# Kernel tuning notes

Hardware: AMD Instinct MI355X
Metric: run time of the kernel (lower is better)

The kernel has to match this reference:

```python
import jax, jax.numpy as jnp
import numpy as np
from jax import lax

EPS = 1e-7  # keras K.epsilon()
DN = ('NHWC', 'HWIO', 'NHWC')


def _box_avg(z, k):
    """Depthwise k x k box filter with SAME padding, scaled by 1/(k*k*C).
    Matches tf.nn.depthwise_conv2d with a ones/(k*k*C) kernel, implemented
    separably (two 1D convs) for efficiency."""
    C = z.shape[-1]
    scale = 1.0 / (k * k * C)  # note: keras code divides by full kernel size incl. C
    kh = jnp.ones((k, 1, 1, C), z.dtype)
    kw = jnp.ones((1, k, 1, C), z.dtype)
    z = lax.conv_general_dilated(z, kh, (1, 1), 'SAME',
                                 dimension_numbers=DN, feature_group_count=C)
    z = lax.conv_general_dilated(z, kw, (1, 1), 'SAME',
                                 dimension_numbers=DN, feature_group_count=C)
    return z * scale


def setup_inputs() -> dict:
    key = jax.random.key(0)
    x = jax.random.normal(key, (8, 1024, 1024, 2), dtype=jnp.float32)
    return {"x": x, "filter_size": 61}


def reference(x, filter_size):
    k = int(filter_size)
    # norm_method == 'std':
    out = x - _box_avg(x, k)                       # local mean-subtract
    c1 = _box_avg(out, k)
    c2 = _box_avg(out * out, k)
    std = jnp.sqrt(c2 - c1 * c1) + EPS             # local window std
    return out / std
```

## Files before the change

### kernel.cpp

```cpp
#include <hip/hip_runtime.h>
#include <math.h>

#define NB 8
#define HH 1024
#define WW 1024
#define RAD 30
#define KS 61
#define ROWSZ 2048
#define IMGSZ (HH * ROWSZ)
#define STR2 1024
#define NCOL2 (NB * STR2)
#define VSEGH 32
#define VNSEG (HH / VSEGH)
#define EPSV 1e-7f
#define SCALEV (1.0f / (float)(KS * KS * 2))
#define PDW (WW + WW / 8)
#define PD(i) ((i) + ((i) >> 3))

__device__ __forceinline__ unsigned bf16_rn(float f) {
    unsigned u = __float_as_uint(f);
    return (u + 0x7FFFu + ((u >> 16) & 1u)) >> 16;
}
__device__ __forceinline__ unsigned pk2(float a, float b) {
    return bf16_rn(a) | (bf16_rn(b) << 16);
}
__device__ __forceinline__ float2 up2(unsigned u) {
    return make_float2(__uint_as_float(u << 16),
                       __uint_as_float(u & 0xFFFF0000u));
}

__device__ __forceinline__ float2 f2add(float2 a, float2 b) {
    return make_float2(a.x + b.x, a.y + b.y);
}
__device__ __forceinline__ float2 f2sub(float2 a, float2 b) {
    return make_float2(a.x - b.x, a.y - b.y);
}

__global__ __launch_bounds__(256, 2) void vbox_kernel(const float* __restrict__ in,
                                                      unsigned* __restrict__ out) {
    int tid = blockIdx.x * 256 + threadIdx.x;
    int col = tid & (NCOL2 - 1);
    int seg = tid >> 13;
    int n = col >> 10;
    int w2 = col & (STR2 - 1);
    const float2* ip = (const float2*)(in + (size_t)n * IMGSZ) + w2;
    unsigned* op = out + (size_t)n * (IMGSZ / 2) + w2;
    int h0 = seg * VSEGH;
    float2 S = make_float2(0.f, 0.f);
    int lo = h0 - RAD; if (lo < 0) lo = 0;
    int h = lo;
    for (; h + 8 <= h0 + RAD; h += 8) {
        float2 W[8];
        #pragma unroll
        for (int i = 0; i < 8; ++i) W[i] = ip[(h + i) * STR2];
        __builtin_amdgcn_sched_barrier(0);
        #pragma unroll
        for (int i = 0; i < 8; ++i) S = f2add(S, W[i]);
    }
    for (; h < h0 + RAD; ++h) S = f2add(S, ip[h * STR2]);

    if (seg != 0 && seg != VNSEG - 1) {
        const float2* lp = ip + (h0 + RAD) * STR2;
        const float2* tp = ip + (h0 - RAD) * STR2;
        unsigned* opp = op + (size_t)h0 * STR2;
        for (int r = 0; r < VSEGH; r += 8) {
            float2 L[8], T[8];
            #pragma unroll
            for (int i = 0; i < 8; ++i) L[i] = lp[(r + i) * STR2];
            #pragma unroll
            for (int i = 0; i < 8; ++i) T[i] = tp[(r + i) * STR2];
            __builtin_amdgcn_sched_barrier(0);
            #pragma unroll
            for (int i = 0; i < 8; ++i) {
                S = f2add(S, L[i]);
                opp[(r + i) * STR2] = pk2(S.x, S.y);
                S = f2sub(S, T[i]);
            }
        }
    } else {
        const float2 Z = make_float2(0.f, 0.f);
        for (int ho = h0; ho < h0 + VSEGH; ho += 4) {
            float2 a[4], b[4];
            #pragma unroll
            for (int i = 0; i < 4; ++i) {
                int ha = ho + i + RAD;
                a[i] = (ha < HH) ? ip[ha * STR2] : Z;
            }
            #pragma unroll
            for (int i = 0; i < 4; ++i) {
                int hb = ho + i - RAD;
                b[i] = (hb >= 0) ? ip[hb * STR2] : Z;
            }
            #pragma unroll
            for (int i = 0; i < 4; ++i) {
                S = f2add(S, a[i]);
                op[(size_t)(ho + i) * STR2] = pk2(S.x, S.y);
                S = f2sub(S, b[i]);
            }
        }
    }
}

__device__ inline float wave_incl_scan(float v) {
    int lane = threadIdx.x & 63;
    #pragma unroll
    for (int d = 1; d < 64; d <<= 1) {
        float o = __shfl_up(v, d, 64);
        if (lane >= d) v += o;
    }
    return v;
}

__global__ __launch_bounds__(256) void hmid_kernel(const unsigned* __restrict__ vsum,
                                                   const float* __restrict__ x,
                                                   float* __restrict__ out,
                                                   uint2* __restrict__ hig) {
    __shared__ float ch[2][PDW];
    __shared__ float s4[4][PDW];
    __shared__ float wtot[4];
    int t = threadIdx.x;
    size_t g = (size_t)blockIdx.x * ROWSZ;
    const uint4* vrow = (const uint4*)(vsum + (size_t)blockIdx.x * STR2);
    uint4 u = vrow[t];
    {
        float2 p0 = up2(u.x), p1 = up2(u.y), p2 = up2(u.z), p3 = up2(u.w);
        int w = 4 * t;
        ch[0][PD(w + 0)] = p0.x; ch[1][PD(w + 0)] = p0.y;
        ch[0][PD(w + 1)] = p1.x; ch[1][PD(w + 1)] = p1.y;
        ch[0][PD(w + 2)] = p2.x; ch[1][PD(w + 2)] = p2.y;
        ch[0][PD(w + 3)] = p3.x; ch[1][PD(w + 3)] = p3.y;
    }
    __syncthreads();
    {
        int c = t >> 7, j = t & 127, base = j * 8;
        float v[8]; float run = 0.f;
        #pragma unroll
        for (int i = 0; i < 8; ++i) { run += ch[c][PD(base + i)]; v[i] = run; }
        float incl = wave_incl_scan(run);
        int wid = t >> 6;
        if ((t & 63) == 63) wtot[wid] = incl;
        __syncthreads();
        float off = incl - run;
        if (wid & 1) off += wtot[wid - 1];
        #pragma unroll
        for (int i = 0; i < 8; ++i) ch[c][PD(base + i)] = off + v[i];
    }
    __syncthreads();
    const float4* xrow = (const float4*)(x + g);
    float4* orow = (float4*)(out + g);
    #pragma unroll
    for (int i = 0; i < 2; ++i) {
        int jj = t + 256 * i;
        int w0 = 2 * jj, w1 = 2 * jj + 1;
        int hi0 = w0 + RAD; if (hi0 > WW - 1) hi0 = WW - 1;
        int hi1 = w1 + RAD; if (hi1 > WW - 1) hi1 = WW - 1;
        int lo0 = w0 - RAD - 1, lo1 = w1 - RAD - 1;
        float s00 = ch[0][PD(hi0)], s10 = ch[1][PD(hi0)];
        if (lo0 >= 0) { s00 -= ch[0][PD(lo0)]; s10 -= ch[1][PD(lo0)]; }
        float s01 = ch[0][PD(hi1)], s11 = ch[1][PD(hi1)];
        if (lo1 >= 0) { s01 -= ch[0][PD(lo1)]; s11 -= ch[1][PD(lo1)]; }
        float4 xv = xrow[jj];
        float4 o;
        o.x = xv.x - SCALEV * s00; o.y = xv.y - SCALEV * s10;
        o.z = xv.z - SCALEV * s01; o.w = xv.w - SCALEV * s11;
        orow[jj] = o;
        s4[0][PD(w0)] = o.x;       s4[1][PD(w0)] = o.y;
        s4[0][PD(w1)] = o.z;       s4[1][PD(w1)] = o.w;
        s4[2][PD(w0)] = o.x * o.x; s4[3][PD(w0)] = o.y * o.y;
        s4[2][PD(w1)] = o.z * o.z; s4[3][PD(w1)] = o.w * o.w;
    }
    __syncthreads();
    {
        int a = t >> 6, j = t & 63, base = j * 16;
        float v[16]; float run = 0.f;
        #pragma unroll
        for (int i = 0; i < 16; ++i) { run += s4[a][PD(base + i)]; v[i] = run; }
        float incl = wave_incl_scan(run);
        float off = incl - run;
        #pragma unroll
        for (int i = 0; i < 16; ++i) s4[a][PD(base + i)] = off + v[i];
    }
    __syncthreads();
    uint4* hirow = (uint4*)(hig + (size_t)blockIdx.x * STR2);
    #pragma unroll
    for (int i = 0; i < 2; ++i) {
        int jj = t + 256 * i;
        int w0 = 2 * jj, w1 = 2 * jj + 1;
        int hi0 = w0 + RAD; if (hi0 > WW - 1) hi0 = WW - 1;
        int hi1 = w1 + RAD; if (hi1 > WW - 1) hi1 = WW - 1;
        int lo0 = w0 - RAD - 1, lo1 = w1 - RAD - 1;
        float a00 = s4[0][PD(hi0)], a10 = s4[1][PD(hi0)];
        float q00 = s4[2][PD(hi0)], q10 = s4[3][PD(hi0)];
        if (lo0 >= 0) {
            a00 -= s4[0][PD(lo0)]; a10 -= s4[1][PD(lo0)];
            q00 -= s4[2][PD(lo0)]; q10 -= s4[3][PD(lo0)];
        }
        float a01 = s4[0][PD(hi1)], a11 = s4[1][PD(hi1)];
        float q01 = s4[2][PD(hi1)], q11 = s4[3][PD(hi1)];
        if (lo1 >= 0) {
            a01 -= s4[0][PD(lo1)]; a11 -= s4[1][PD(lo1)];
            q01 -= s4[2][PD(lo1)]; q11 -= s4[3][PD(lo1)];
        }
        hirow[jj] = make_uint4(pk2(a00, a10), pk2(q00, q10),
                               pk2(a01, a11), pk2(q01, q11));
    }
}

__global__ __launch_bounds__(256, 2) void vfinal_kernel(const uint2* __restrict__ hi,
                                                        float* __restrict__ io) {
    int tid = blockIdx.x * 256 + threadIdx.x;
    int col = tid & (NCOL2 - 1);
    int seg = tid >> 13;
    int n = col >> 10;
    int w2 = col & (STR2 - 1);
    const uint2* pp = hi + (size_t)n * ((size_t)HH * STR2) + w2;
    float2* op = (float2*)(io + (size_t)n * IMGSZ) + w2;
    int h0 = seg * VSEGH;
    float2 S1 = make_float2(0.f, 0.f);
    float2 S2 = make_float2(0.f, 0.f);
    int lo = h0 - RAD; if (lo < 0) lo = 0;
    int h = lo;
    for (; h + 8 <= h0 + RAD; h += 8) {
        uint2 A[8];
        #pragma unroll
        for (int i = 0; i < 8; ++i) A[i] = pp[(h + i) * STR2];
        __builtin_amdgcn_sched_barrier(0);
        #pragma unroll
        for (int i = 0; i < 8; ++i) {
            S1 = f2add(S1, up2(A[i].x));
            S2 = f2add(S2, up2(A[i].y));
        }
    }
    for (; h < h0 + RAD; ++h) {
        uint2 v = pp[h * STR2];
        S1 = f2add(S1, up2(v.x));
        S2 = f2add(S2, up2(v.y));
    }

    if (seg != 0 && seg != VNSEG - 1) {
        const uint2* lp = pp + (h0 + RAD) * STR2;
        const uint2* tp = pp + (h0 - RAD) * STR2;
        float2* q = op + (size_t)h0 * STR2;
        for (int r = 0; r < VSEGH; r += 8) {
            uint2 L[8], T[8];
            float2 O[8];
            #pragma unroll
            for (int i = 0; i < 8; ++i) L[i] = lp[(r + i) * STR2];
            #pragma unroll
            for (int i = 0; i < 8; ++i) T[i] = tp[(r + i) * STR2];
            #pragma unroll
            for (int i = 0; i < 8; ++i) O[i] = q[(r + i) * STR2];
            __builtin_amdgcn_sched_barrier(0);
            #pragma unroll
            for (int i = 0; i < 8; ++i) {
                S1 = f2add(S1, up2(L[i].x));
                S2 = f2add(S2, up2(L[i].y));
                float c1x = SCALEV * S1.x, c1y = SCALEV * S1.y;
                float vx = fmaxf(SCALEV * S2.x - c1x * c1x, 0.f);
                float vy = fmaxf(SCALEV * S2.y - c1y * c1y, 0.f);
                float2 yv;
                yv.x = O[i].x / (sqrtf(vx) + EPSV);
                yv.y = O[i].y / (sqrtf(vy) + EPSV);
                q[(r + i) * STR2] = yv;
                S1 = f2sub(S1, up2(T[i].x));
                S2 = f2sub(S2, up2(T[i].y));
            }
        }
    } else {
        const uint2 Z2u = make_uint2(0u, 0u);
        for (int ho = h0; ho < h0 + VSEGH; ho += 4) {
            uint2 a[4], b[4];
            float2 O[4];
            #pragma unroll
            for (int i = 0; i < 4; ++i) {
                int ha = ho + i + RAD;
                a[i] = (ha < HH) ? pp[ha * STR2] : Z2u;
            }
            #pragma unroll
            for (int i = 0; i < 4; ++i) {
                int hb = ho + i - RAD;
                b[i] = (hb >= 0) ? pp[hb * STR2] : Z2u;
            }
            #pragma unroll
            for (int i = 0; i < 4; ++i) O[i] = op[(size_t)(ho + i) * STR2];
            #pragma unroll
            for (int i = 0; i < 4; ++i) {
                S1 = f2add(S1, up2(a[i].x));
                S2 = f2add(S2, up2(a[i].y));
                float c1x = SCALEV * S1.x, c1y = SCALEV * S1.y;
                float vx = fmaxf(SCALEV * S2.x - c1x * c1x, 0.f);
                float vy = fmaxf(SCALEV * S2.y - c1y * c1y, 0.f);
                float2 yv;
                yv.x = O[i].x / (sqrtf(vx) + EPSV);
                yv.y = O[i].y / (sqrtf(vy) + EPSV);
                op[(size_t)(ho + i) * STR2] = yv;
                S1 = f2sub(S1, up2(b[i].x));
                S2 = f2sub(S2, up2(b[i].y));
            }
        }
    }
}

extern "C" void kernel_launch(void* const* d_in, const int* in_sizes, int n_in,
                              void* d_out, int out_size, void* d_ws, size_t ws_size,
                              hipStream_t stream) {
    const float* x = (const float*)d_in[0];
    float* out = (float*)d_out;
    unsigned* V1 = (unsigned*)d_ws;
    uint2* HI = (uint2*)(V1 + (size_t)NB * IMGSZ / 2);

    int vgrid = (NCOL2 * VNSEG) / 256;
    vbox_kernel<<<vgrid, 256, 0, stream>>>(x, V1);
    hmid_kernel<<<NB * HH, 256, 0, stream>>>(V1, x, out, HI);
    vfinal_kernel<<<vgrid, 256, 0, stream>>>(HI, out);
}
```

Measured before the change: 208.9 us.

## Widen vertical box kernels to 16-byte accesses with double-buffered row loads

Both vertical running-sum kernels now handle two pixels (four channels) per thread using float4/uint4 loads and stores instead of 8-byte accesses, which halves the thread count. The interior path double-buffers 8-row batches so the next batch's loads are in flight while the current one is consumed. The final kernel also swaps the divide and sqrtf for the hardware rcp/sqrt builtins. The cost is more registers (launch_bounds minimum occupancy hint dropped) and fewer waves in flight, plus slightly lower precision from the approximate rcp/sqrt.

```diff
diff --git a/kernel.cpp b/kernel.cpp
--- a/kernel.cpp
+++ b/kernel.cpp
@@ -9,7 +9,8 @@
 #define ROWSZ 2048
 #define IMGSZ (HH * ROWSZ)
 #define STR2 1024
-#define NCOL2 (NB * STR2)
+#define STR4 512
+#define NCOL4 (NB * STR4)
 #define VSEGH 32
 #define VNSEG (HH / VSEGH)
 #define EPSV 1e-7f
@@ -28,74 +29,86 @@
     return make_float2(__uint_as_float(u << 16),
                        __uint_as_float(u & 0xFFFF0000u));
 }
-
 __device__ __forceinline__ float2 f2add(float2 a, float2 b) {
     return make_float2(a.x + b.x, a.y + b.y);
 }
 __device__ __forceinline__ float2 f2sub(float2 a, float2 b) {
     return make_float2(a.x - b.x, a.y - b.y);
 }
-
-__global__ __launch_bounds__(256, 2) void vbox_kernel(const float* __restrict__ in,
-                                                      unsigned* __restrict__ out) {
+__device__ __forceinline__ float sqrt_f(float x) { return __builtin_amdgcn_sqrtf(x); }
+__device__ __forceinline__ float rcp_f(float x)  { return __builtin_amdgcn_rcpf(x); }
+
+__global__ __launch_bounds__(256) void vbox_kernel(const float* __restrict__ in,
+                                                   unsigned* __restrict__ out) {
     int tid = blockIdx.x * 256 + threadIdx.x;
-    int col = tid & (NCOL2 - 1);
-    int seg = tid >> 13;
-    int n = col >> 10;
-    int w2 = col & (STR2 - 1);
-    const float2* ip = (const float2*)(in + (size_t)n * IMGSZ) + w2;
-    unsigned* op = out + (size_t)n * (IMGSZ / 2) + w2;
+    int col = tid & (NCOL4 - 1);
+    int seg = tid >> 12;
+    int n = col >> 9;
+    int c = col & (STR4 - 1);
+    const float4* ip = (const float4*)(in + (size_t)n * IMGSZ) + c;
+    uint2* op = (uint2*)(out + (size_t)n * (IMGSZ / 2)) + c;
     int h0 = seg * VSEGH;
-    float2 S = make_float2(0.f, 0.f);
+    float4 S = make_float4(0.f, 0.f, 0.f, 0.f);
     int lo = h0 - RAD; if (lo < 0) lo = 0;
     int h = lo;
     for (; h + 8 <= h0 + RAD; h += 8) {
-        float2 W[8];
-        #pragma unroll
-        for (int i = 0; i < 8; ++i) W[i] = ip[(h + i) * STR2];
+        float4 W[8];
+        #pragma unroll
+        for (int i = 0; i < 8; ++i) W[i] = ip[(h + i) * STR4];
         __builtin_amdgcn_sched_barrier(0);
         #pragma unroll
-        for (int i = 0; i < 8; ++i) S = f2add(S, W[i]);
-    }
-    for (; h < h0 + RAD; ++h) S = f2add(S, ip[h * STR2]);
+        for (int i = 0; i < 8; ++i) {
+            S.x += W[i].x; S.y += W[i].y; S.z += W[i].z; S.w += W[i].w;
+        }
+    }
+    for (; h < h0 + RAD; ++h) {
+        float4 w = ip[h * STR4];
+        S.x += w.x; S.y += w.y; S.z += w.z; S.w += w.w;
+    }
 
     if (seg != 0 && seg != VNSEG - 1) {
-        const float2* lp = ip + (h0 + RAD) * STR2;
-        const float2* tp = ip + (h0 - RAD) * STR2;
-        unsigned* opp = op + (size_t)h0 * STR2;
-        for (int r = 0; r < VSEGH; r += 8) {
-            float2 L[8], T[8];
-            #pragma unroll
-            for (int i = 0; i < 8; ++i) L[i] = lp[(r + i) * STR2];
-            #pragma unroll
-            for (int i = 0; i < 8; ++i) T[i] = tp[(r + i) * STR2];
-            __builtin_amdgcn_sched_barrier(0);
-            #pragma unroll
-            for (int i = 0; i < 8; ++i) {
-                S = f2add(S, L[i]);
-                opp[(r + i) * STR2] = pk2(S.x, S.y);
-                S = f2sub(S, T[i]);
-            }
-        }
+        const float4* lp = ip + (h0 + RAD) * STR4;
+        const float4* tp = ip + (h0 - RAD) * STR4;
+        uint2* opp = op + (size_t)h0 * STR4;
+        float4 LA[8], TA[8], LB[8], TB[8];
+#define VB_LOAD(Lx, Tx, r) { \
+        _Pragma("unroll") for (int i = 0; i < 8; ++i) Lx[i] = lp[((r) + i) * STR4]; \
+        _Pragma("unroll") for (int i = 0; i < 8; ++i) Tx[i] = tp[((r) + i) * STR4]; \
+        __builtin_amdgcn_sched_barrier(0); }
+#define VB_CONS(Lx, Tx, r) { \
+        _Pragma("unroll") for (int i = 0; i < 8; ++i) { \
+            S.x += Lx[i].x; S.y += Lx[i].y; S.z += Lx[i].z; S.w += Lx[i].w; \
+            opp[((r) + i) * STR4] = make_uint2(pk2(S.x, S.y), pk2(S.z, S.w)); \
+            S.x -= Tx[i].x; S.y -= Tx[i].y; S.z -= Tx[i].z; S.w -= Tx[i].w; } }
+        VB_LOAD(LA, TA, 0)
+        VB_LOAD(LB, TB, 8)
+        VB_CONS(LA, TA, 0)
+        VB_LOAD(LA, TA, 16)
+        VB_CONS(LB, TB, 8)
+        VB_LOAD(LB, TB, 24)
+        VB_CONS(LA, TA, 16)
+        VB_CONS(LB, TB, 24)
+#undef VB_LOAD
+#undef VB_CONS
     } else {
-        const float2 Z = make_float2(0.f, 0.f);
+        const float4 Z = make_float4(0.f, 0.f, 0.f, 0.f);
         for (int ho = h0; ho < h0 + VSEGH; ho += 4) {
-            float2 a[4], b[4];
+            float4 a[4], b[4];
             #pragma unroll
             for (int i = 0; i < 4; ++i) {
                 int ha = ho + i + RAD;
-                a[i] = (ha < HH) ? ip[ha * STR2] : Z;
+                a[i] = (ha < HH) ? ip[ha * STR4] : Z;
             }
             #pragma unroll
             for (int i = 0; i < 4; ++i) {
                 int hb = ho + i - RAD;
-                b[i] = (hb >= 0) ? ip[hb * STR2] : Z;
-            }
-            #pragma unroll
-            for (int i = 0; i < 4; ++i) {
-                S = f2add(S, a[i]);
-                op[(size_t)(ho + i) * STR2] = pk2(S.x, S.y);
-                S = f2sub(S, b[i]);
+                b[i] = (hb >= 0) ? ip[hb * STR4] : Z;
+            }
+            #pragma unroll
+            for (int i = 0; i < 4; ++i) {
+                S.x += a[i].x; S.y += a[i].y; S.z += a[i].z; S.w += a[i].w;
+                op[(size_t)(ho + i) * STR4] = make_uint2(pk2(S.x, S.y), pk2(S.z, S.w));
+                S.x -= b[i].x; S.y -= b[i].y; S.z -= b[i].z; S.w -= b[i].w;
             }
         }
     }
@@ -206,99 +219,99 @@
     }
 }
 
-__global__ __launch_bounds__(256, 2) void vfinal_kernel(const uint2* __restrict__ hi,
-                                                        float* __restrict__ io) {
+__global__ __launch_bounds__(256) void vfinal_kernel(const uint2* __restrict__ hi,
+                                                     float* __restrict__ io) {
     int tid = blockIdx.x * 256 + threadIdx.x;
-    int col = tid & (NCOL2 - 1);
-    int seg = tid >> 13;
-    int n = col >> 10;
-    int w2 = col & (STR2 - 1);
-    const uint2* pp = hi + (size_t)n * ((size_t)HH * STR2) + w2;
-    float2* op = (float2*)(io + (size_t)n * IMGSZ) + w2;
+    int col = tid & (NCOL4 - 1);
+    int seg = tid >> 12;
+    int n = col >> 9;
+    int c = col & (STR4 - 1);
+    const uint4* pp = (const uint4*)(hi + (size_t)n * (size_t)HH * STR2) + c;
+    float4* op = (float4*)(io + (size_t)n * IMGSZ) + c;
     int h0 = seg * VSEGH;
-    float2 S1 = make_float2(0.f, 0.f);
-    float2 S2 = make_float2(0.f, 0.f);
+    float2 S1a = make_float2(0.f, 0.f), S2a = make_float2(0.f, 0.f);
+    float2 S1b = make_float2(0.f, 0.f), S2b = make_float2(0.f, 0.f);
     int lo = h0 - RAD; if (lo < 0) lo = 0;
     int h = lo;
     for (; h + 8 <= h0 + RAD; h += 8) {
-        uint2 A[8];
-        #pragma unroll
-        for (int i = 0; i < 8; ++i) A[i] = pp[(h + i) * STR2];
+        uint4 A[8];
+        #pragma unroll
+        for (int i = 0; i < 8; ++i) A[i] = pp[(h + i) * STR4];
         __builtin_amdgcn_sched_barrier(0);
         #pragma unroll
         for (int i = 0; i < 8; ++i) {
-            S1 = f2add(S1, up2(A[i].x));
-            S2 = f2add(S2, up2(A[i].y));
+            S1a = f2add(S1a, up2(A[i].x)); S2a = f2add(S2a, up2(A[i].y));
+            S1b = f2add(S1b, up2(A[i].z)); S2b = f2add(S2b, up2(A[i].w));
         }
     }
     for (; h < h0 + RAD; ++h) {
-        uint2 v = pp[h * STR2];
-        S1 = f2add(S1, up2(v.x));
-        S2 = f2add(S2, up2(v.y));
-    }
+        uint4 v = pp[h * STR4];
+        S1a = f2add(S1a, up2(v.x)); S2a = f2add(S2a, up2(v.y));
+        S1b = f2add(S1b, up2(v.z)); S2b = f2add(S2b, up2(v.w));
+    }
+
+#define VF_ROW(Ai, Oi, Ti, ro) { \
+    S1a = f2add(S1a, up2((Ai).x)); S2a = f2add(S2a, up2((Ai).y)); \
+    S1b = f2add(S1b, up2((Ai).z)); S2b = f2add(S2b, up2((Ai).w)); \
+    float4 yv; \
+    yv.x = (Oi).x * rcp_f(sqrt_f(fmaxf(SCALEV * S2a.x - (SCALEV * S1a.x) * (SCALEV * S1a.x), 0.f)) + EPSV); \
+    yv.y = (Oi).y * rcp_f(sqrt_f(fmaxf(SCALEV * S2a.y - (SCALEV * S1a.y) * (SCALEV * S1a.y), 0.f)) + EPSV); \
+    yv.z = (Oi).z * rcp_f(sqrt_f(fmaxf(SCALEV * S2b.x - (SCALEV * S1b.x) * (SCALEV * S1b.x), 0.f)) + EPSV); \
+    yv.w = (Oi).w * rcp_f(sqrt_f(fmaxf(SCALEV * S2b.y - (SCALEV * S1b.y) * (SCALEV * S1b.y), 0.f)) + EPSV); \
+    oq[(ro) * STR4] = yv; \
+    S1a = f2sub(S1a, up2((Ti).x)); S2a = f2sub(S2a, up2((Ti).y)); \
+    S1b = f2sub(S1b, up2((Ti).z)); S2b = f2sub(S2b, up2((Ti).w)); \
+}
 
     if (seg != 0 && seg != VNSEG - 1) {
-        const uint2* lp = pp + (h0 + RAD) * STR2;
-        const uint2* tp = pp + (h0 - RAD) * STR2;
-        float2* q = op + (size_t)h0 * STR2;
-        for (int r = 0; r < VSEGH; r += 8) {
-            uint2 L[8], T[8];
-            float2 O[8];
-            #pragma unroll
-            for (int i = 0; i < 8; ++i) L[i] = lp[(r + i) * STR2];
-            #pragma unroll
-            for (int i = 0; i < 8; ++i) T[i] = tp[(r + i) * STR2];
-            #pragma unroll
-            for (int i = 0; i < 8; ++i) O[i] = q[(r + i) * STR2];
-            __builtin_amdgcn_sched_barrier(0);
-            #pragma unroll
-            for (int i = 0; i < 8; ++i) {
-                S1 = f2add(S1, up2(L[i].x));
-                S2 = f2add(S2, up2(L[i].y));
-                float c1x = SCALEV * S1.x, c1y = SCALEV * S1.y;
-                float vx = fmaxf(SCALEV * S2.x - c1x * c1x, 0.f);
-                float vy = fmaxf(SCALEV * S2.y - c1y * c1y, 0.f);
-                float2 yv;
-                yv.x = O[i].x / (sqrtf(vx) + EPSV);
-                yv.y = O[i].y / (sqrtf(vy) + EPSV);
-                q[(r + i) * STR2] = yv;
-                S1 = f2sub(S1, up2(T[i].x));
-                S2 = f2sub(S2, up2(T[i].y));
-            }
-        }
+        const uint4* lp = pp + (h0 + RAD) * STR4;
+        const uint4* tp = pp + (h0 - RAD) * STR4;
+        float4* oq = op + (size_t)h0 * STR4;
+        uint4 LA[8], TA[8], LB[8], TB[8];
+        float4 OA[8], OB[8];
+#define VF_LOAD(Lx, Tx, Ox, r) { \
+        _Pragma("unroll") for (int i = 0; i < 8; ++i) Lx[i] = lp[((r) + i) * STR4]; \
+        _Pragma("unroll") for (int i = 0; i < 8; ++i) Tx[i] = tp[((r) + i) * STR4]; \
+        _Pragma("unroll") for (int i = 0; i < 8; ++i) Ox[i] = oq[((r) + i) * STR4]; \
+        __builtin_amdgcn_sched_barrier(0); }
+#define VF_CONS(Lx, Tx, Ox, r) { \
+        _Pragma("unroll") for (int i = 0; i < 8; ++i) VF_ROW(Lx[i], Ox[i], Tx[i], (r) + i) }
+        VF_LOAD(LA, TA, OA, 0)
+        VF_LOAD(LB, TB, OB, 8)
+        VF_CONS(LA, TA, OA, 0)
+        VF_LOAD(LA, TA, OA, 16)
+        VF_CONS(LB, TB, OB, 8)
+        VF_LOAD(LB, TB, OB, 24)
+        VF_CONS(LA, TA, OA, 16)
+        VF_CONS(LB, TB, OB, 24)
+#undef VF_LOAD
+#undef VF_CONS
     } else {
-        const uint2 Z2u = make_uint2(0u, 0u);
+        const uint4 Z4 = make_uint4(0u, 0u, 0u, 0u);
+        float4* oq = op;
         for (int ho = h0; ho < h0 + VSEGH; ho += 4) {
-            uint2 a[4], b[4];
-            float2 O[4];
+            uint4 a[4], b[4];
+            float4 O[4];
             #pragma unroll
             for (int i = 0; i < 4; ++i) {
                 int ha = ho + i + RAD;
-                a[i] = (ha < HH) ? pp[ha * STR2] : Z2u;
+                a[i] = (ha < HH) ? pp[ha * STR4] : Z4;
             }
             #pragma unroll
             for (int i = 0; i < 4; ++i) {
                 int hb = ho + i - RAD;
-                b[i] = (hb >= 0) ? pp[hb * STR2] : Z2u;
-            }
-            #pragma unroll
-            for (int i = 0; i < 4; ++i) O[i] = op[(size_t)(ho + i) * STR2];
-            #pragma unroll
-            for (int i = 0; i < 4; ++i) {
-                S1 = f2add(S1, up2(a[i].x));
-                S2 = f2add(S2, up2(a[i].y));
-                float c1x = SCALEV * S1.x, c1y = SCALEV * S1.y;
-                float vx = fmaxf(SCALEV * S2.x - c1x * c1x, 0.f);
-                float vy = fmaxf(SCALEV * S2.y - c1y * c1y, 0.f);
-                float2 yv;
-                yv.x = O[i].x / (sqrtf(vx) + EPSV);
-                yv.y = O[i].y / (sqrtf(vy) + EPSV);
-                op[(size_t)(ho + i) * STR2] = yv;
-                S1 = f2sub(S1, up2(b[i].x));
-                S2 = f2sub(S2, up2(b[i].y));
-            }
-        }
-    }
+                b[i] = (hb >= 0) ? pp[hb * STR4] : Z4;
+            }
+            #pragma unroll
+            for (int i = 0; i < 4; ++i) O[i] = op[(size_t)(ho + i) * STR4];
+            #pragma unroll
+            for (int i = 0; i < 4; ++i) {
+                VF_ROW(a[i], O[i], b[i], (size_t)(ho + i))
+            }
+        }
+        (void)oq;
+    }
+#undef VF_ROW
 }
 
 extern "C" void kernel_launch(void* const* d_in, const int* in_sizes, int n_in,
@@ -309,7 +322,7 @@
     unsigned* V1 = (unsigned*)d_ws;
     uint2* HI = (uint2*)(V1 + (size_t)NB * IMGSZ / 2);
 
-    int vgrid = (NCOL2 * VNSEG) / 256;
+    int vgrid = (NCOL4 * VNSEG) / 256;
     vbox_kernel<<<vgrid, 256, 0, stream>>>(x, V1);
     hmid_kernel<<<NB * HH, 256, 0, stream>>>(V1, x, out, HI);
     vfinal_kernel<<<vgrid, 256, 0, stream>>>(HI, out);
```

New measurement: 209.7 us. No clear change (+0.4%).
